# Kernel optimization log

Measured on AMD Instinct MI355X. Metric: run time of the kernel, lower is better.

Reference implementation:

```python
import jax, jax.numpy as jnp
import numpy as np

D_IN, H, V = 512, 1024, 32000
S, B, T = 64, 128, 48
MARGIN = 0.1


def setup_inputs() -> dict:
    key = jax.random.key(0)
    ks = jax.random.split(key, 16)
    sc = 0.05
    f = lambda k, shp: jax.random.normal(k, shp, jnp.float32) * sc
    emb_W = f(ks[0], (V, D_IN)).at[0].set(0.0)  # padding_idx=0 row is zero
    return dict(
        ctx=jax.random.normal(ks[1], (S, B, H), jnp.float32),
        ctx_mask=jnp.ones((S, B), jnp.float32),
        y=jax.random.randint(ks[2], (T, B), 0, V),
        emb_W=emb_W,
        W_init=f(ks[3], (H, H)), b_init=jnp.zeros((H,), jnp.float32),
        W_ih0=f(ks[4], (3 * H, D_IN)), W_hh0=f(ks[5], (3 * H, H)),
        b_ih0=jnp.zeros((3 * H,), jnp.float32), b_hh0=jnp.zeros((3 * H,), jnp.float32),
        W_c2c=f(ks[6], (H, H)), W_h2c=f(ks[7], (H, H)), v_att=f(ks[8], (H,)),
        W_ih1=f(ks[9], (3 * H, H)), W_hh1=f(ks[10], (3 * H, H)),
        b_ih1=jnp.zeros((3 * H,), jnp.float32), b_hh1=jnp.zeros((3 * H,), jnp.float32),
        W_h2o=f(ks[11], (D_IN, H)), b_h2o=jnp.zeros((D_IN,), jnp.float32),
        W_out=f(ks[12], (V, D_IN)),
    )


def _gru(x, h, Wih, Whh, bih, bhh):
    # torch.nn.GRUCell math
    gi = x @ Wih.T + bih
    gh = h @ Whh.T + bhh
    ir, iz, inn = jnp.split(gi, 3, axis=-1)
    hr, hz, hn = jnp.split(gh, 3, axis=-1)
    r = jax.nn.sigmoid(ir + hr)
    z = jax.nn.sigmoid(iz + hz)
    n = jnp.tanh(inn + r * hn)
    return (1.0 - z) * n + z * h


def reference(ctx, ctx_mask, y, emb_W, W_init, b_init, W_ih0, W_hh0, b_ih0, b_hh0,
              W_c2c, W_h2c, v_att, W_ih1, W_hh1, b_ih1, b_hh1, W_h2o, b_h2o, W_out):
    # dec_init='mean_ctx': tanh(FF(masked mean over source))
    mean_ctx = ctx.sum(0) / ctx_mask.sum(0)[:, None]            # (B,H)
    h = jnp.tanh(mean_ctx @ W_init.T + b_init)                  # h0 (B,H)

    ctx_p = jnp.einsum('sbc,dc->sbd', ctx, W_c2c)               # ctx2ctx, hoisted out of loop
    neg = jnp.where(ctx_mask > 0, 0.0, -1e9)                    # (S,B) additive mask
    W_out_n = W_out / jnp.linalg.norm(W_out, axis=-1, keepdims=True)

    emb_in = emb_W[y[:-1]]                                      # (T-1,B,D_IN)
    targets = y[1:]                                             # (T-1,B)

    def step(h, inp):
        e, tgt = inp
        h1 = _gru(e, h, W_ih0, W_hh0, b_ih0, b_hh0)             # dec0
        # MLP attention: v^T tanh(ctx2ctx(ctx) + hid2ctx(h1))
        scores = jnp.tanh(ctx_p + (h1 @ W_h2c.T)[None]) @ v_att + neg   # (S,B)
        alpha = jax.nn.softmax(scores, axis=0)
        z_t = jnp.einsum('sb,sbc->bc', alpha, ctx)              # context (B,H)
        h2 = _gru(z_t, h1, W_ih1, W_hh1, b_ih1, b_hh1)          # dec1
        logit = jnp.tanh(h2 @ W_h2o.T + b_h2o)                  # hid2out
        logit = logit / jnp.linalg.norm(logit, axis=-1, keepdims=True)
        log_p = logit @ W_out_n.T                               # (B,V) cosine sims
        # max-margin loss, contrastive_type='max', ignore pad (tgt==0)
        s_true = jnp.take_along_axis(log_p, tgt[:, None], axis=1)
        viol = jnp.maximum(MARGIN - s_true + log_p, 0.0)
        viol = viol * (1.0 - jax.nn.one_hot(tgt, V, dtype=log_p.dtype))
        l = jnp.sum(jnp.where(tgt != 0, viol.max(-1), 0.0))
        return h2, l

    _, losses = jax.lax.scan(step, h, (emb_in, targets))
    return losses.sum()
```

## Files before the change

### kernel.cpp

```cpp
#include <hip/hip_runtime.h>
#include <math.h>

#define H    1024
#define H3   3072
#define DIN  512
#define VSZ  32000
#define SS   64
#define BB   128
#define TP   47
#define NROWS (TP*BB)
#define VCHUNKS 250
#define FMARGIN 0.1f
#define NBLK 256
#define HS   65536
#define PS(i) ((i) + ((i) >> 4))

typedef unsigned short u16;
typedef unsigned int u32;
typedef unsigned long long u64;
typedef __bf16 bf16_t;
typedef bf16_t bf16x8 __attribute__((ext_vector_type(8)));
typedef float f32x4 __attribute__((ext_vector_type(4)));
typedef u16 u16x4 __attribute__((ext_vector_type(4)));
typedef u16 u16x8 __attribute__((ext_vector_type(8)));

#define MFMA __builtin_amdgcn_mfma_f32_16x16x32_bf16

__device__ inline u16 f2bf(float f){
    unsigned b = __float_as_uint(f);
    return (u16)((b + 0x7FFFu + ((b >> 16) & 1u)) >> 16);
}
__device__ inline float bf2f(u16 u){ return __uint_as_float(((unsigned)u) << 16); }
__device__ inline float sigm(float x){ return 1.f/(1.f + expf(-x)); }

__device__ inline void stoval(float* p, float v){ *p = v; }
__device__ inline void stoval(u16* p, float v){ *p = f2bf(v); }

__device__ inline void cstore(u32* p, u32 v){ __hip_atomic_store(p, v, __ATOMIC_RELAXED, __HIP_MEMORY_SCOPE_AGENT); }
__device__ inline void cstore64(u64* p, u64 v){ __hip_atomic_store(p, v, __ATOMIC_RELAXED, __HIP_MEMORY_SCOPE_AGENT); }
__device__ inline float cloadf(const float* p){ return __hip_atomic_load(p, __ATOMIC_RELAXED, __HIP_MEMORY_SCOPE_AGENT); }

__device__ inline void gbar(u32* bar, u32* mygen, int tid, int bid){
    __syncthreads();
    if (tid == 0){
        u32 tgt = ++(*mygen);
        __builtin_amdgcn_s_waitcnt(0);
        u32* cnt = bar + 64 + (bid >> 3)*32;
        u32 old = __hip_atomic_fetch_add(cnt, 1u, __ATOMIC_RELAXED, __HIP_MEMORY_SCOPE_AGENT);
        if (old == 7u){
            __hip_atomic_store(cnt, 0u, __ATOMIC_RELAXED, __HIP_MEMORY_SCOPE_AGENT);
            u32 old2 = __hip_atomic_fetch_add(&bar[1], 1u, __ATOMIC_RELEASE, __HIP_MEMORY_SCOPE_AGENT);
            if (old2 == 31u){
                __hip_atomic_store(&bar[1], 0u, __ATOMIC_RELAXED, __HIP_MEMORY_SCOPE_AGENT);
                __hip_atomic_store(&bar[0], tgt, __ATOMIC_RELEASE, __HIP_MEMORY_SCOPE_AGENT);
            }
        }
        while (__hip_atomic_load(&bar[0], __ATOMIC_RELAXED, __HIP_MEMORY_SCOPE_AGENT) < tgt)
            __builtin_amdgcn_s_sleep(1);
    }
    __syncthreads();
    asm volatile("" ::: "memory");
}


__global__ __launch_bounds__(128) void k_mask_sum(const float* __restrict__ mask, float* __restrict__ msum){
    int b = threadIdx.x;
    if (b < BB){ float s = 0.f; for (int i = 0; i < SS; i++) s += mask[i*BB + b]; msum[b] = s; }
}

__global__ __launch_bounds__(256) void k_mean_ctx(const float* __restrict__ ctx, const float* __restrict__ msum,
                                                  float* __restrict__ mean){
    int idx = blockIdx.x*256 + threadIdx.x;
    if (idx < BB*H){
        float s = 0.f;
        for (int i = 0; i < SS; i++) s += ctx[(size_t)i*BB*H + idx];
        mean[idx] = s / msum[idx / H];
    }
}

__global__ __launch_bounds__(256) void k_f32bf(const float* __restrict__ in, u16* __restrict__ out, int n4){
    int i = blockIdx.x*256 + threadIdx.x;
    if (i >= n4) return;
    float4 v = ((const float4*)in)[i];
    u16x4 o = { f2bf(v.x), f2bf(v.y), f2bf(v.z), f2bf(v.w) };
    ((u16x4*)out)[i] = o;
}

__global__ __launch_bounds__(256) void k_pack_h0(const float* __restrict__ h0, u32* __restrict__ hsHI,
                                                 u32* __restrict__ hsLO){
    int i = blockIdx.x*256 + threadIdx.x;
    float v0 = h0[i*2], v1 = h0[i*2 + 1];
    u16 a = f2bf(v0), b = f2bf(v1);
    hsHI[i] = (u32)a | ((u32)b << 16);
    hsLO[i] = (u32)f2bf(v0 - bf2f(a)) | ((u32)f2bf(v1 - bf2f(b)) << 16);
}

__global__ __launch_bounds__(256) void k_f2bf_frag(const float* __restrict__ in, u16* __restrict__ out,
                                                   int RK8, int K8){
    int t = blockIdx.x*256 + threadIdx.x;
    if (t >= RK8) return;
    int r = t / K8, k8 = t - r*K8;
    const float* p = in + (size_t)r*K8*8 + k8*8;
    float4 a = *(const float4*)p;
    float4 b = *(const float4*)(p + 4);
    size_t dst = ((size_t)(r >> 4)*(K8 >> 2) + (k8 >> 2))*512 + (size_t)((r & 15) + (k8 & 3)*16)*8;
    u16x8 o;
    o[0]=f2bf(a.x); o[1]=f2bf(a.y); o[2]=f2bf(a.z); o[3]=f2bf(a.w);
    o[4]=f2bf(b.x); o[5]=f2bf(b.y); o[6]=f2bf(b.z); o[7]=f2bf(b.w);
    *(u16x8*)(out + dst) = o;
}

__global__ __launch_bounds__(256) void k_rownorm_frag(const float* __restrict__ in, u16* __restrict__ out,
                                                      int nrows){
    int w = threadIdx.x >> 6, lane = threadIdx.x & 63;
    int row = blockIdx.x*4 + w;
    if (row >= nrows) return;
    const float* r = in + (size_t)row*512 + lane*8;
    float4 a = *(const float4*)r;
    float4 b = *(const float4*)(r + 4);
    float s = a.x*a.x + a.y*a.y + a.z*a.z + a.w*a.w
            + b.x*b.x + b.y*b.y + b.z*b.z + b.w*b.w;
    #pragma unroll
    for (int off = 32; off; off >>= 1) s += __shfl_xor(s, off);
    float inv = rsqrtf(s);
    size_t dst = ((size_t)(row >> 4)*16 + (lane >> 2))*512 + (size_t)((row & 15) + (lane & 3)*16)*8;
    u16x8 o;
    o[0]=f2bf(a.x*inv); o[1]=f2bf(a.y*inv); o[2]=f2bf(a.z*inv); o[3]=f2bf(a.w*inv);
    o[4]=f2bf(b.x*inv); o[5]=f2bf(b.y*inv); o[6]=f2bf(b.z*inv); o[7]=f2bf(b.w*inv);
    *(u16x8*)(out + dst) = o;
}

__global__ __launch_bounds__(256) void k_emb_frag(const float* __restrict__ emb, const int* __restrict__ y,
                                                  u16* __restrict__ out){
    int w = threadIdx.x >> 6, lane = threadIdx.x & 63;
    int row = blockIdx.x*4 + w;
    int src = y[row];
    const float* r = emb + (size_t)src*512 + lane*8;
    float4 a = *(const float4*)r;
    float4 b = *(const float4*)(r + 4);
    size_t dst = ((size_t)(row >> 4)*16 + (lane >> 2))*512 + (size_t)((row & 15) + (lane & 3)*16)*8;
    u16x8 o;
    o[0]=f2bf(a.x); o[1]=f2bf(a.y); o[2]=f2bf(a.z); o[3]=f2bf(a.w);
    o[4]=f2bf(b.x); o[5]=f2bf(b.y); o[6]=f2bf(b.z); o[7]=f2bf(b.w);
    *(u16x8*)(out + dst) = o;
}

template<int ACT>
__global__ __launch_bounds__(256) void k_gemm_nt(const float* __restrict__ A, const float* __restrict__ W,
                                                 const float* __restrict__ bias, float* __restrict__ C,
                                                 int M, int N, int K){
    __shared__ float As[16][68];
    __shared__ float Ws[16][68];
    int tid = threadIdx.x;
    int bm = blockIdx.y*64, bn = blockIdx.x*64;
    int lr = tid >> 2;
    int lk = (tid & 3) * 4;
    int tr = (tid >> 4) * 4;
    int tc = (tid & 15) * 4;
    float acc[4][4] = {};
    const float* Abase = A + (size_t)(bm + lr)*K;
    const float* Wbase = W + (size_t)(bn + lr)*K;
    for (int k0 = 0; k0 < K; k0 += 16){
        float4 av = *(const float4*)(Abase + k0 + lk);
        float4 wv = *(const float4*)(Wbase + k0 + lk);
        __syncthreads();
        As[lk+0][lr]=av.x; As[lk+1][lr]=av.y; As[lk+2][lr]=av.z; As[lk+3][lr]=av.w;
        Ws[lk+0][lr]=wv.x; Ws[lk+1][lr]=wv.y; Ws[lk+2][lr]=wv.z; Ws[lk+3][lr]=wv.w;
        __syncthreads();
        #pragma unroll
        for (int kk = 0; kk < 16; kk++){
            float4 a = *(const float4*)&As[kk][tr];
            float4 w = *(const float4*)&Ws[kk][tc];
            acc[0][0] += a.x*w.x; acc[0][1] += a.x*w.y; acc[0][2] += a.x*w.z; acc[0][3] += a.x*w.w;
            acc[1][0] += a.y*w.x; acc[1][1] += a.y*w.y; acc[1][2] += a.y*w.z; acc[1][3] += a.y*w.w;
            acc[2][0] += a.z*w.x; acc[2][1] += a.z*w.y; acc[2][2] += a.z*w.z; acc[2][3] += a.z*w.w;
            acc[3][0] += a.w*w.x; acc[3][1] += a.w*w.y; acc[3][2] += a.w*w.z; acc[3][3] += a.w*w.w;
        }
    }
    #pragma unroll
    for (int i = 0; i < 4; i++){
        #pragma unroll
        for (int j = 0; j < 4; j++){
            float v = acc[i][j];
            if (bias) v += bias[bn + tc + j];
            if (ACT == 1) v = tanhf(v);
            C[(size_t)(bm + tr + i)*N + bn + tc + j] = v;
        }
    }
}

template<int AFRAG, int ACT, typename OutT>
__global__ __launch_bounds__(256) void k_gemmf(const u16* __restrict__ A, const u16* __restrict__ B,
                                               const float* __restrict__ bias, OutT* __restrict__ C,
                                               int M, int N, int K){
    int tid = threadIdx.x, lane = tid & 63, w = tid >> 6;
    int wm = w >> 1, wn = w & 1;
    int row0 = blockIdx.y*128 + wm*64, col0 = blockIdx.x*128 + wn*64;
    int r16 = lane & 15, kg8 = (lane >> 4)*8, rg = (lane >> 4)*4;
    int K32 = K >> 5;
    f32x4 acc[4][4] = {};
    for (int k0 = 0; k0 < K32; k0++){
        bf16x8 af[4], bfv[4];
        #pragma unroll
        for (int i = 0; i < 4; i++){
            if (AFRAG) af[i] = *(const bf16x8*)(A + (((size_t)((row0 >> 4) + i)*K32 + k0) << 9) + lane*8);
            else       af[i] = *(const bf16x8*)(A + (size_t)(row0 + i*16 + r16)*K + k0*32 + kg8);
        }
        #pragma unroll
        for (int j = 0; j < 4; j++)
            bfv[j] = *(const bf16x8*)(B + (((size_t)((col0 >> 4) + j)*K32 + k0) << 9) + lane*8);
        #pragma unroll
        for (int i = 0; i < 4; i++)
            #pragma unroll
            for (int j = 0; j < 4; j++)
                acc[i][j] = MFMA(af[i], bfv[j], acc[i][j], 0, 0, 0);
    }
    #pragma unroll
    for (int i = 0; i < 4; i++){
        #pragma unroll
        for (int j = 0; j < 4; j++){
            #pragma unroll
            for (int r = 0; r < 4; r++){
                int row = row0 + i*16 + rg + r;
                int col = col0 + j*16 + r16;
                float v = acc[i][j][r];
                if (bias) v += bias[col];
                if (ACT) v = tanhf(v);
                stoval(C + (size_t)row*N + col, v);
            }
        }
    }
}

struct RH {
    const u16 *gi0, *Whh0, *Wh2c, *Wih1, *Whh1, *ctxp;
    const float *bhh0, *bih1, *bhh1, *vatt, *mask, *ctxf;
    u32 *hsHI, *hsLO, *h1HI, *h1LO, *ztHI, *ztLO;
    float *prF;
    float *ghF;
    u16 *h2all;
    u32 *bar;
};

__global__ __launch_bounds__(512) void k_recur7(RH a){
    __shared__ u16 wlds[49152];
    __shared__ float ps[1088];
    __shared__ float vattL[1088];
    __shared__ float sal[SS];
    __shared__ float zred[4][512];
    const int tid = threadIdx.x, lane = tid & 63, wv = tid >> 6;
    const int bid = blockIdx.x;
    const int r16 = lane & 15, rg = (lane >> 4)*4, kq4 = (lane >> 4)*4;
    const int ab = (bid & 7)*16 + ((bid >> 3) >> 1);
    const int ahalf = (bid >> 3) & 1;
    u32 mygen = 0;

    {
        auto cp32k = [&](const u16* gsrc, int tile, int base){
            const u32* s = (const u32*)(gsrc + (size_t)tile*16384);
            u32* d = (u32*)(wlds + base);
            #pragma unroll
            for (int i = 0; i < 16; i++) d[tid + i*512] = s[tid + i*512];
        };
        if (bid < 64){
            cp32k(a.Whh0, bid, 0); cp32k(a.Whh0, 64+bid, 16384); cp32k(a.Whh0, 128+bid, 32768);
        } else if (bid < 128){
            int jt = bid - 64;
            cp32k(a.Wih1, jt, 0); cp32k(a.Wih1, 64+jt, 16384); cp32k(a.Wih1, 128+jt, 32768);
        } else if (bid < 192){
            int wt = bid - 128;
            cp32k(a.Whh1, 3*wt, 0); cp32k(a.Whh1, 3*wt+1, 16384); cp32k(a.Whh1, 3*wt+2, 32768);
        } else {
            cp32k(a.Wh2c, bid-192, 0);
        }
        for (int i = tid; i < H; i += 512) vattL[PS(i)] = a.vatt[i];
    }
    __syncthreads();

    auto pf_ctxp = [&](){
        u32 acc = 0;
        #pragma unroll
        for (int i = 0; i < 4; i++){
            int line = tid + i*512;
            int s = line >> 5, l = line & 31;
            acc += *((const u32*)(a.ctxp + ((size_t)(s*BB + ab))*H) + l*16);
        }
        asm volatile("" :: "v"(acc));
    };

    for (int t = 0; t < TP; t++){
        float* prT = a.prF + (size_t)t*BB*H;

        if (bid < 64){
            const u32* AbH = a.hsHI + (size_t)t*HS + (size_t)(wv*16 + r16)*512 + kq4;
            const u32* AbL = a.hsLO + (size_t)t*HS + (size_t)(wv*16 + r16)*512 + kq4;
            f32x4 ac0 = {}, ac1 = {}, ac2 = {};
            for (int k0 = 0; k0 < 32; k0++){
                bf16x8 ah = *(const bf16x8*)(AbH + k0*16);
                bf16x8 al = *(const bf16x8*)(AbL + k0*16);
                bf16x8 b0 = *(const bf16x8*)(wlds + (k0*64 + lane)*8);
                bf16x8 b1 = *(const bf16x8*)(wlds + 16384 + (k0*64 + lane)*8);
                bf16x8 b2 = *(const bf16x8*)(wlds + 32768 + (k0*64 + lane)*8);
                ac0 = MFMA(ah, b0, ac0, 0, 0, 0); ac0 = MFMA(al, b0, ac0, 0, 0, 0);
                ac1 = MFMA(ah, b1, ac1, 0, 0, 0); ac1 = MFMA(al, b1, ac1, 0, 0, 0);
                ac2 = MFMA(ah, b2, ac2, 0, 0, 0); ac2 = MFMA(al, b2, ac2, 0, 0, 0);
            }
            const u16* gi = a.gi0 + (size_t)t*BB*H3;
            const u32* hsH = a.hsHI + (size_t)t*HS;
            const u32* hsL = a.hsLO + (size_t)t*HS;
            int sh = (r16 & 1)*16;
            #pragma unroll
            for (int r = 0; r < 4; r++){
                int b = wv*16 + rg + r, j = bid*16 + r16;
                float gr = bf2f(gi[(size_t)b*H3 + j]);
                float gz = bf2f(gi[(size_t)b*H3 + H + j]);
                float gn = bf2f(gi[(size_t)b*H3 + 2*H + j]);
                float hr = ac0[r] + a.bhh0[j];
                float hz = ac1[r] + a.bhh0[H + j];
                float hn = ac2[r] + a.bhh0[2*H + j];
                u32 uh = hsH[(size_t)b*512 + (j >> 1)];
                u32 ul = hsL[(size_t)b*512 + (j >> 1)];
                float hp = bf2f((u16)(uh >> sh)) + bf2f((u16)(ul >> sh));
                float rr = sigm(gr + hr), zz = sigm(gz + hz);
                float nn = tanhf(gn + rr*hn);
                float hv = (1.f - zz)*nn + zz*hp;
                u16 hib = f2bf(hv);
                u16 lob = f2bf(hv - bf2f(hib));
                u32 hip = (u32)__shfl_xor((int)(u32)hib, 1);
                u32 lop = (u32)__shfl_xor((int)(u32)lob, 1);
                if (!(r16 & 1)){
                    cstore(a.h1HI + (size_t)t*HS + (size_t)b*512 + (j >> 1), (u32)hib | (hip << 16));
                    cstore(a.h1LO + (size_t)t*HS + (size_t)b*512 + (j >> 1), (u32)lob | (lop << 16));
                }
            }
        } else {
            pf_ctxp();
        }
        gbar(a.bar, &mygen, tid, bid);

        if (bid >= 128){
            const u32* AbH = a.h1HI + (size_t)t*HS + (size_t)(wv*16 + r16)*512 + kq4;
            const u32* AbL = a.h1LO + (size_t)t*HS + (size_t)(wv*16 + r16)*512 + kq4;
            if (bid < 192){
                int wt = bid - 128;
                f32x4 ac0 = {}, ac1 = {}, ac2 = {};
                for (int k0 = 0; k0 < 32; k0++){
                    bf16x8 ah = *(const bf16x8*)(AbH + k0*16);
                    bf16x8 al = *(const bf16x8*)(AbL + k0*16);
                    bf16x8 b0 = *(const bf16x8*)(wlds + (k0*64 + lane)*8);
                    bf16x8 b1 = *(const bf16x8*)(wlds + 16384 + (k0*64 + lane)*8);
                    bf16x8 b2 = *(const bf16x8*)(wlds + 32768 + (k0*64 + lane)*8);
                    ac0 = MFMA(ah, b0, ac0, 0, 0, 0); ac0 = MFMA(al, b0, ac0, 0, 0, 0);
                    ac1 = MFMA(ah, b1, ac1, 0, 0, 0); ac1 = MFMA(al, b1, ac1, 0, 0, 0);
                    ac2 = MFMA(ah, b2, ac2, 0, 0, 0); ac2 = MFMA(al, b2, ac2, 0, 0, 0);
                }
                #pragma unroll
                for (int r = 0; r < 4; r++){
                    int b = wv*16 + rg + r;
                    int c0 = wt*48 + r16;
                    float p0 = __shfl_xor(ac0[r], 1);
                    float p1 = __shfl_xor(ac1[r], 1);
                    float p2 = __shfl_xor(ac2[r], 1);
                    if (!(r16 & 1)){
                        cstore64((u64*)(a.ghF + (size_t)b*H3 + c0),
                                 (u64)__float_as_uint(ac0[r]) | ((u64)__float_as_uint(p0) << 32));
                        cstore64((u64*)(a.ghF + (size_t)b*H3 + c0 + 16),
                                 (u64)__float_as_uint(ac1[r]) | ((u64)__float_as_uint(p1) << 32));
                        cstore64((u64*)(a.ghF + (size_t)b*H3 + c0 + 32),
                                 (u64)__float_as_uint(ac2[r]) | ((u64)__float_as_uint(p2) << 32));
                    }
                }
            } else {
                f32x4 ac = {};
                for (int k0 = 0; k0 < 32; k0++){
                    bf16x8 ah = *(const bf16x8*)(AbH + k0*16);
                    bf16x8 al = *(const bf16x8*)(AbL + k0*16);
                    bf16x8 bv = *(const bf16x8*)(wlds + (k0*64 + lane)*8);
                    ac = MFMA(ah, bv, ac, 0, 0, 0); ac = MFMA(al, bv, ac, 0, 0, 0);
                }
                #pragma unroll
                for (int r = 0; r < 4; r++){
                    int b = wv*16 + rg + r;
                    int c0 = (bid - 192)*16 + r16;
                    float p0 = __shfl_xor(ac[r], 1);
                    if (!(r16 & 1))
                        cstore64((u64*)(prT + (size_t)b*H + c0),
                                 (u64)__float_as_uint(ac[r]) | ((u64)__float_as_uint(p0) << 32));
                }
            }
        } else if (bid < 64){
            pf_ctxp();
        }
        gbar(a.bar, &mygen, tid, bid);

        {
            int b = ab;
            for (int i = tid; i < H; i += 512) ps[PS(i)] = prT[(size_t)b*H + i];
            __syncthreads();
            #pragma unroll
            for (int q = 0; q < 8; q += 2){
                int s0 = wv*8 + q, s1 = s0 + 1;
                const u16* cpA = a.ctxp + ((size_t)(s0*BB + b))*H + lane*16;
                const u16* cpB = a.ctxp + ((size_t)(s1*BB + b))*H + lane*16;
                u16x8 a0 = *(const u16x8*)cpA;
                u16x8 a1 = *(const u16x8*)(cpA + 8);
                u16x8 b0 = *(const u16x8*)cpB;
                u16x8 b1 = *(const u16x8*)(cpB + 8);
                const float* pp = ps + lane*17;
                const float* vv = vattL + lane*17;
                float accA = 0.f, accB = 0.f;
                #pragma unroll
                for (int e = 0; e < 8; e++){
                    accA += tanhf(bf2f(a0[e]) + pp[e]) * vv[e];
                    accB += tanhf(bf2f(b0[e]) + pp[e]) * vv[e];
                }
                #pragma unroll
                for (int e = 0; e < 8; e++){
                    accA += tanhf(bf2f(a1[e]) + pp[8 + e]) * vv[8 + e];
                    accB += tanhf(bf2f(b1[e]) + pp[8 + e]) * vv[8 + e];
                }
                #pragma unroll
                for (int off = 32; off; off >>= 1){
                    accA += __shfl_xor(accA, off);
                    accB += __shfl_xor(accB, off);
                }
                if (lane == 0){
                    sal[s0] = accA + ((a.mask[s0*BB + b] > 0.f) ? 0.f : -1e9f);
                    sal[s1] = accB + ((a.mask[s1*BB + b] > 0.f) ? 0.f : -1e9f);
                }
            }
            __syncthreads();
            if (tid < 64){
                float v = sal[tid];
                float m = v;
                #pragma unroll
                for (int off = 32; off; off >>= 1) m = fmaxf(m, __shfl_xor(m, off));
                float e = expf(v - m);
                float su = e;
                #pragma unroll
                for (int off = 32; off; off >>= 1) su += __shfl_xor(su, off);
                sal[tid] = e / su;
            }
            __syncthreads();
            int cq = (tid & 127)*4, sg = tid >> 7;
            float4 z = {0.f, 0.f, 0.f, 0.f};
            #pragma unroll
            for (int so = 0; so < 16; so += 4){
                float4 c0 = *(const float4*)(a.ctxf + ((size_t)((sg + (so+0)*4)*BB + b))*H + ahalf*512 + cq);
                float4 c1 = *(const float4*)(a.ctxf + ((size_t)((sg + (so+1)*4)*BB + b))*H + ahalf*512 + cq);
                float4 c2 = *(const float4*)(a.ctxf + ((size_t)((sg + (so+2)*4)*BB + b))*H + ahalf*512 + cq);
                float4 c3 = *(const float4*)(a.ctxf + ((size_t)((sg + (so+3)*4)*BB + b))*H + ahalf*512 + cq);
                float l0 = sal[sg + (so+0)*4], l1 = sal[sg + (so+1)*4];
                float l2 = sal[sg + (so+2)*4], l3 = sal[sg + (so+3)*4];
                z.x += l0*c0.x + l1*c1.x + l2*c2.x + l3*c3.x;
                z.y += l0*c0.y + l1*c1.y + l2*c2.y + l3*c3.y;
                z.z += l0*c0.z + l1*c1.z + l2*c2.z + l3*c3.z;
                z.w += l0*c0.w + l1*c1.w + l2*c2.w + l3*c3.w;
            }
            *(float4*)&zred[sg][cq] = z;
            __syncthreads();
            if (tid < 256){
                int c2 = tid*2;
                float a0 = zred[0][c2]   + zred[1][c2]   + zred[2][c2]   + zred[3][c2];
                float a1 = zred[0][c2+1] + zred[1][c2+1] + zred[2][c2+1] + zred[3][c2+1];
                int j0 = ahalf*512 + c2;
                u16 z0 = f2bf(a0), z1 = f2bf(a1);
                cstore(a.ztHI + (size_t)t*HS + (size_t)b*512 + (j0 >> 1), (u32)z0 | ((u32)z1 << 16));
                cstore(a.ztLO + (size_t)t*HS + (size_t)b*512 + (j0 >> 1),
                       (u32)f2bf(a0 - bf2f(z0)) | ((u32)f2bf(a1 - bf2f(z1)) << 16));
            }
            __syncthreads();
        }
        gbar(a.bar, &mygen, tid, bid);

        if (bid >= 64 && bid < 128){
            int jt = bid - 64;
            const u32* AbH = a.ztHI + (size_t)t*HS + (size_t)(wv*16 + r16)*512 + kq4;
            const u32* AbL = a.ztLO + (size_t)t*HS + (size_t)(wv*16 + r16)*512 + kq4;
            f32x4 ac0 = {}, ac1 = {}, ac2 = {};
            for (int k0 = 0; k0 < 32; k0++){
                bf16x8 ah = *(const bf16x8*)(AbH + k0*16);
                bf16x8 al = *(const bf16x8*)(AbL + k0*16);
                bf16x8 b0 = *(const bf16x8*)(wlds + (k0*64 + lane)*8);
                bf16x8 b1 = *(const bf16x8*)(wlds + 16384 + (k0*64 + lane)*8);
                bf16x8 b2 = *(const bf16x8*)(wlds + 32768 + (k0*64 + lane)*8);
                ac0 = MFMA(ah, b0, ac0, 0, 0, 0); ac0 = MFMA(al, b0, ac0, 0, 0, 0);
                ac1 = MFMA(ah, b1, ac1, 0, 0, 0); ac1 = MFMA(al, b1, ac1, 0, 0, 0);
                ac2 = MFMA(ah, b2, ac2, 0, 0, 0); ac2 = MFMA(al, b2, ac2, 0, 0, 0);
            }
            const u32* h1H = a.h1HI + (size_t)t*HS;
            const u32* h1L = a.h1LO + (size_t)t*HS;
            int sh = (r16 & 1)*16;
            #pragma unroll
            for (int r = 0; r < 4; r++){
                int b = wv*16 + rg + r, j = jt*16 + r16;
                float gr = ac0[r] + a.bih1[j];
                float gz = ac1[r] + a.bih1[H + j];
                float gn = ac2[r] + a.bih1[2*H + j];
                float hr = cloadf(a.ghF + (size_t)b*H3 + j)       + a.bhh1[j];
                float hz = cloadf(a.ghF + (size_t)b*H3 + H + j)   + a.bhh1[H + j];
                float hn = cloadf(a.ghF + (size_t)b*H3 + 2*H + j) + a.bhh1[2*H + j];
                u32 uh = h1H[(size_t)b*512 + (j >> 1)];
                u32 ul = h1L[(size_t)b*512 + (j >> 1)];
                float h1v = bf2f((u16)(uh >> sh)) + bf2f((u16)(ul >> sh));
                float rr = sigm(gr + hr), zz = sigm(gz + hz);
                float nn = tanhf(gn + rr*hn);
                float hv = (1.f - zz)*nn + zz*h1v;
                a.h2all[((size_t)t*BB + b)*H + j] = f2bf(hv);
                u16 hib = f2bf(hv);
                u16 lob = f2bf(hv - bf2f(hib));
                u32 hip = (u32)__shfl_xor((int)(u32)hib, 1);
                u32 lop = (u32)__shfl_xor((int)(u32)lob, 1);
                if (!(r16 & 1)){
                    cstore(a.hsHI + (size_t)(t+1)*HS + (size_t)b*512 + (j >> 1), (u32)hib | (hip << 16));
                    cstore(a.hsLO + (size_t)(t+1)*HS + (size_t)b*512 + (j >> 1), (u32)lob | (lop << 16));
                }
            }
        }
        gbar(a.bar, &mygen, tid, bid);
    }
}

__global__ __launch_bounds__(256) void k_final(const u16* __restrict__ logitf, const u16* __restrict__ Wf,
                                               const int* __restrict__ y, float* __restrict__ pmax,
                                               float* __restrict__ strue){
    __shared__ float red[128][2];
    int tid = threadIdx.x, w = tid >> 6, lane = tid & 63;
    int wm = w >> 1, wn = w & 1;
    int row0 = blockIdx.x*128 + wm*64;
    int col0 = blockIdx.y*128 + wn*64;
    int r16 = lane & 15, rg = (lane >> 4)*4;
    f32x4 acc[4][4] = {};
    for (int k0 = 0; k0 < 16; k0++){
        bf16x8 af[4], bfv[4];
        #pragma unroll
        for (int i = 0; i < 4; i++)
            af[i] = *(const bf16x8*)(logitf + (((size_t)((row0 >> 4) + i)*16 + k0) << 9) + lane*8);
        #pragma unroll
        for (int j = 0; j < 4; j++)
            bfv[j] = *(const bf16x8*)(Wf + (((size_t)((col0 >> 4) + j)*16 + k0) << 9) + lane*8);
        #pragma unroll
        for (int i = 0; i < 4; i++)
            #pragma unroll
            for (int j = 0; j < 4; j++)
                acc[i][j] = MFMA(af[i], bfv[j], acc[i][j], 0, 0, 0);
    }
    #pragma unroll
    for (int i = 0; i < 4; i++){
        #pragma unroll
        for (int r = 0; r < 4; r++){
            int row = row0 + i*16 + rg + r;
            int tgt = y[row + BB];
            float m = -1e30f;
            #pragma unroll
            for (int j = 0; j < 4; j++){
                float v = acc[i][j][r];
                int col = col0 + j*16 + r16;
                if (col == tgt){ strue[row] = v; v = -1e30f; }
                m = fmaxf(m, v);
            }
            m = fmaxf(m, __shfl_xor(m, 1));
            m = fmaxf(m, __shfl_xor(m, 2));
            m = fmaxf(m, __shfl_xor(m, 4));
            m = fmaxf(m, __shfl_xor(m, 8));
            if (r16 == 0) red[wm*64 + i*16 + rg + r][wn] = m;
        }
    }
    __syncthreads();
    if (tid < 128){
        float m = fmaxf(red[tid][0], red[tid][1]);
        pmax[(size_t)(blockIdx.x*128 + tid)*VCHUNKS + blockIdx.y] = m;
    }
}

__global__ __launch_bounds__(256) void k_loss(const float* __restrict__ pmax, const float* __restrict__ strue,
                                              const int* __restrict__ y, float* __restrict__ out){
    int R = blockIdx.x*256 + threadIdx.x;
    int lane = threadIdx.x & 63, wave = threadIdx.x >> 6;
    float l = 0.f;
    if (R < NROWS){
        int tgt = y[R + BB];
        if (tgt != 0){
            const float* pm = pmax + (size_t)R*VCHUNKS;
            float m = -1e30f;
            for (int i = 0; i < VCHUNKS; i++) m = fmaxf(m, pm[i]);
            l = fmaxf(FMARGIN - strue[R] + m, 0.f);
        }
    }
    #pragma unroll
    for (int off = 32; off; off >>= 1) l += __shfl_down(l, off);
    __shared__ float wsum[4];
    if (lane == 0) wsum[wave] = l;
    __syncthreads();
    if (threadIdx.x == 0) atomicAdd(out, wsum[0] + wsum[1] + wsum[2] + wsum[3]);
}

extern "C" void kernel_launch(void* const* d_in, const int* in_sizes, int n_in,
                              void* d_out, int out_size, void* d_ws, size_t ws_size,
                              hipStream_t stream){
    const float* ctx    = (const float*)d_in[0];
    const float* mask   = (const float*)d_in[1];
    const int*   y      = (const int*)d_in[2];
    const float* emb_W  = (const float*)d_in[3];
    const float* W_init = (const float*)d_in[4];
    const float* b_init = (const float*)d_in[5];
    const float* W_ih0  = (const float*)d_in[6];
    const float* W_hh0  = (const float*)d_in[7];
    const float* b_ih0  = (const float*)d_in[8];
    const float* b_hh0  = (const float*)d_in[9];
    const float* W_c2c  = (const float*)d_in[10];
    const float* W_h2c  = (const float*)d_in[11];
    const float* v_att  = (const float*)d_in[12];
    const float* W_ih1  = (const float*)d_in[13];
    const float* W_hh1  = (const float*)d_in[14];
    const float* b_ih1  = (const float*)d_in[15];
    const float* b_hh1  = (const float*)d_in[16];
    const float* W_h2o  = (const float*)d_in[17];
    const float* b_h2o  = (const float*)d_in[18];
    const float* W_out  = (const float*)d_in[19];
    float* out = (float*)d_out;

    char* wsb = (char*)d_ws;
    size_t off = 0;
    auto alloc = [&](size_t bytes)->void*{
        void* p = (void*)(wsb + off);
        off = (off + bytes + 255) & ~(size_t)255;
        return p;
    };
    u16* Wih0f = (u16*)alloc((size_t)H3*DIN*2);
    u16* Whh0f = (u16*)alloc((size_t)H3*H*2);
    u16* Wih1f = (u16*)alloc((size_t)H3*H*2);
    u16* Whh1f = (u16*)alloc((size_t)H3*H*2);
    u16* Wh2cf = (u16*)alloc((size_t)H*H*2);
    u16* Wc2cf = (u16*)alloc((size_t)H*H*2);
    u16* Wh2of = (u16*)alloc((size_t)DIN*H*2);
    u16* Woutf = (u16*)alloc((size_t)VSZ*DIN*2);
    u16* ctxb  = (u16*)alloc((size_t)SS*BB*H*2);
    u16* ctxpb = (u16*)alloc((size_t)SS*BB*H*2);
    u16* embf  = (u16*)alloc((size_t)NROWS*DIN*2);
    u16* gi0b  = (u16*)alloc((size_t)NROWS*H3*2);
    u16* h2allb= (u16*)alloc((size_t)NROWS*H*2);
    u32* hsHI  = (u32*)alloc((size_t)(TP+1)*HS*4);
    u32* hsLO  = (u32*)alloc((size_t)(TP+1)*HS*4);
    u32* h1HI  = (u32*)alloc((size_t)TP*HS*4);
    u32* h1LO  = (u32*)alloc((size_t)TP*HS*4);
    u32* ztHI  = (u32*)alloc((size_t)TP*HS*4);
    u32* ztLO  = (u32*)alloc((size_t)TP*HS*4);
    float* ghF = (float*)alloc((size_t)BB*H3*4);
    u32* bar   = (u32*)alloc(8192);
    float* strue  = (float*)alloc(NROWS*4);
    float* msum   = (float*)alloc(BB*4);
    float* meanc  = (float*)alloc((size_t)BB*H*4);
    float* h0f    = (float*)alloc((size_t)BB*H*4);

    float* prF = (float*)Woutf;

    float* logitf  = (float*)gi0b;
    u16*   logitfr = (u16*)(gi0b + (size_t)NROWS*DIN*2);
    float* pmax    = (float*)(gi0b + (size_t)NROWS*DIN*2 + (size_t)NROWS*DIN);

    hipMemsetAsync(d_out, 0, sizeof(float), stream);
    hipMemsetAsync(bar, 0, 8192, stream);

    hipLaunchKernelGGL(k_mask_sum, dim3(1), dim3(128), 0, stream, mask, msum);
    hipLaunchKernelGGL(k_mean_ctx, dim3(BB*H/256), dim3(256), 0, stream, ctx, msum, meanc);
    hipLaunchKernelGGL((k_gemm_nt<1>), dim3(H/64, BB/64), dim3(256), 0, stream,
                       meanc, W_init, b_init, h0f, BB, H, H);
    hipLaunchKernelGGL(k_pack_h0, dim3(HS/256), dim3(256), 0, stream, h0f, hsHI, hsLO);

    hipLaunchKernelGGL(k_f2bf_frag, dim3(H3*DIN/8/256), dim3(256), 0, stream, W_ih0, Wih0f, H3*DIN/8, DIN/8);
    hipLaunchKernelGGL(k_f2bf_frag, dim3(H3*H/8/256), dim3(256), 0, stream, W_hh0, Whh0f, H3*H/8, H/8);
    hipLaunchKernelGGL(k_f2bf_frag, dim3(H3*H/8/256), dim3(256), 0, stream, W_ih1, Wih1f, H3*H/8, H/8);
    hipLaunchKernelGGL(k_f2bf_frag, dim3(H3*H/8/256), dim3(256), 0, stream, W_hh1, Whh1f, H3*H/8, H/8);
    hipLaunchKernelGGL(k_f2bf_frag, dim3(H*H/8/256), dim3(256), 0, stream, W_h2c, Wh2cf, H*H/8, H/8);
    hipLaunchKernelGGL(k_f2bf_frag, dim3(H*H/8/256), dim3(256), 0, stream, W_c2c, Wc2cf, H*H/8, H/8);
    hipLaunchKernelGGL(k_f2bf_frag, dim3(DIN*H/8/256), dim3(256), 0, stream, W_h2o, Wh2of, DIN*H/8, H/8);
    hipLaunchKernelGGL(k_f32bf, dim3(SS*BB*H/4/256), dim3(256), 0, stream, ctx, ctxb, SS*BB*H/4);
    hipLaunchKernelGGL(k_emb_frag, dim3(NROWS/4), dim3(256), 0, stream, emb_W, y, embf);

    hipLaunchKernelGGL((k_gemmf<1,0,u16>), dim3(H3/128, NROWS/128), dim3(256), 0, stream,
                       embf, Wih0f, b_ih0, gi0b, NROWS, H3, DIN);
    hipLaunchKernelGGL((k_gemmf<0,0,u16>), dim3(H/128, SS*BB/128), dim3(256), 0, stream,
                       ctxb, Wc2cf, (const float*)nullptr, ctxpb, SS*BB, H, H);

    RH rh;
    rh.gi0 = gi0b; rh.Whh0 = Whh0f; rh.Wh2c = Wh2cf; rh.Wih1 = Wih1f; rh.Whh1 = Whh1f;
    rh.ctxp = ctxpb;
    rh.bhh0 = b_hh0; rh.bih1 = b_ih1; rh.bhh1 = b_hh1; rh.vatt = v_att; rh.mask = mask; rh.ctxf = ctx;
    rh.hsHI = hsHI; rh.hsLO = hsLO; rh.h1HI = h1HI; rh.h1LO = h1LO; rh.ztHI = ztHI; rh.ztLO = ztLO;
    rh.prF = prF; rh.ghF = ghF;
    rh.h2all = h2allb; rh.bar = bar;
    void* kp[] = { (void*)&rh };
    hipLaunchCooperativeKernel((const void*)k_recur7, dim3(NBLK), dim3(512), kp, 0, stream);

    hipLaunchKernelGGL(k_rownorm_frag, dim3(VSZ/4), dim3(256), 0, stream, W_out, Woutf, VSZ);
    hipLaunchKernelGGL((k_gemmf<0,1,float>), dim3(DIN/128, NROWS/128), dim3(256), 0, stream,
                       h2allb, Wh2of, b_h2o, logitf, NROWS, DIN, H);
    hipLaunchKernelGGL(k_rownorm_frag, dim3(NROWS/4), dim3(256), 0, stream, logitf, logitfr, NROWS);
    hipLaunchKernelGGL(k_final, dim3(NROWS/128, VSZ/128), dim3(256), 0, stream,
                       logitfr, Woutf, y, pmax, strue);
    hipLaunchKernelGGL(k_loss, dim3((NROWS + 255)/256), dim3(256), 0, stream, pmax, strue, y, out);
}
```

Measured before the change: 5.978 ms.

## Cache ctx projection slice in LDS and split attention scores across block halves

Each block now keeps its batch element's half-width slice of the projected context in LDS for 62 of 64 source positions, and holds v_att in registers. This replaces re-reading ctx_p from global memory every step and drops the prefetch-warming code. Scores are computed per half (512 columns) and written as partial sums to a global buffer, combined after an extra grid barrier per timestep. The context vector reduction is also simplified to one column per thread over all S. The cost is one more grid-wide barrier per step and more LDS use, which may lower occupancy headroom.

After: 5.126 ms. 14.2% less time.

```diff
diff --git a/kernel.cpp b/kernel.cpp
--- a/kernel.cpp
+++ b/kernel.cpp
@@ -13,7 +13,7 @@
 #define FMARGIN 0.1f
 #define NBLK 256
 #define HS   65536
-#define PS(i) ((i) + ((i) >> 4))
+#define CTXPL_S 62
 
 typedef unsigned short u16;
 typedef unsigned int u32;
@@ -37,6 +37,7 @@
 __device__ inline void stoval(u16* p, float v){ *p = f2bf(v); }
 
 __device__ inline void cstore(u32* p, u32 v){ __hip_atomic_store(p, v, __ATOMIC_RELAXED, __HIP_MEMORY_SCOPE_AGENT); }
+__device__ inline void cstoref(float* p, float v){ __hip_atomic_store(p, v, __ATOMIC_RELAXED, __HIP_MEMORY_SCOPE_AGENT); }
 __device__ inline void cstore64(u64* p, u64 v){ __hip_atomic_store(p, v, __ATOMIC_RELAXED, __HIP_MEMORY_SCOPE_AGENT); }
 __device__ inline float cloadf(const float* p){ return __hip_atomic_load(p, __ATOMIC_RELAXED, __HIP_MEMORY_SCOPE_AGENT); }
 
@@ -232,22 +233,21 @@
     }
 }
 
-struct RH {
+struct RI {
     const u16 *gi0, *Whh0, *Wh2c, *Wih1, *Whh1, *ctxp;
     const float *bhh0, *bih1, *bhh1, *vatt, *mask, *ctxf;
     u32 *hsHI, *hsLO, *h1HI, *h1LO, *ztHI, *ztLO;
     float *prF;
     float *ghF;
+    float *spar;
     u16 *h2all;
     u32 *bar;
 };
 
-__global__ __launch_bounds__(512) void k_recur7(RH a){
+__global__ __launch_bounds__(512) void k_recur8(RI a){
     __shared__ u16 wlds[49152];
-    __shared__ float ps[1088];
-    __shared__ float vattL[1088];
+    __shared__ u16 ctxpL[CTXPL_S*512];
     __shared__ float sal[SS];
-    __shared__ float zred[4][512];
     const int tid = threadIdx.x, lane = tid & 63, wv = tid >> 6;
     const int bid = blockIdx.x;
     const int r16 = lane & 15, rg = (lane >> 4)*4, kq4 = (lane >> 4)*4;
@@ -273,23 +273,23 @@
         } else {
             cp32k(a.Wh2c, bid-192, 0);
         }
-        for (int i = tid; i < H; i += 512) vattL[PS(i)] = a.vatt[i];
+        for (int i = tid; i < CTXPL_S*512/8; i += 512){
+            int s = (i*8) >> 9, h = (i*8) & 511;
+            *(u16x8*)(ctxpL + i*8) = *(const u16x8*)(a.ctxp + ((size_t)(s*BB + ab))*H + ahalf*512 + h);
+        }
+    }
+    float vv[8];
+    {
+        float4 v0 = *(const float4*)(a.vatt + ahalf*512 + lane*8);
+        float4 v1 = *(const float4*)(a.vatt + ahalf*512 + lane*8 + 4);
+        vv[0]=v0.x; vv[1]=v0.y; vv[2]=v0.z; vv[3]=v0.w;
+        vv[4]=v1.x; vv[5]=v1.y; vv[6]=v1.z; vv[7]=v1.w;
     }
     __syncthreads();
-
-    auto pf_ctxp = [&](){
-        u32 acc = 0;
-        #pragma unroll
-        for (int i = 0; i < 4; i++){
-            int line = tid + i*512;
-            int s = line >> 5, l = line & 31;
-            acc += *((const u32*)(a.ctxp + ((size_t)(s*BB + ab))*H) + l*16);
-        }
-        asm volatile("" :: "v"(acc));
-    };
 
     for (int t = 0; t < TP; t++){
         float* prT = a.prF + (size_t)t*BB*H;
+        float* spT = a.spar + (size_t)t*256*SS;
 
         if (bid < 64){
             const u32* AbH = a.hsHI + (size_t)t*HS + (size_t)(wv*16 + r16)*512 + kq4;
@@ -333,8 +333,6 @@
                     cstore(a.h1LO + (size_t)t*HS + (size_t)b*512 + (j >> 1), (u32)lob | (lop << 16));
                 }
             }
-        } else {
-            pf_ctxp();
         }
         gbar(a.bar, &mygen, tid, bid);
 
@@ -388,50 +386,37 @@
                                  (u64)__float_as_uint(ac[r]) | ((u64)__float_as_uint(p0) << 32));
                 }
             }
-        } else if (bid < 64){
-            pf_ctxp();
         }
         gbar(a.bar, &mygen, tid, bid);
 
         {
-            int b = ab;
-            for (int i = tid; i < H; i += 512) ps[PS(i)] = prT[(size_t)b*H + i];
-            __syncthreads();
-            #pragma unroll
-            for (int q = 0; q < 8; q += 2){
-                int s0 = wv*8 + q, s1 = s0 + 1;
-                const u16* cpA = a.ctxp + ((size_t)(s0*BB + b))*H + lane*16;
-                const u16* cpB = a.ctxp + ((size_t)(s1*BB + b))*H + lane*16;
-                u16x8 a0 = *(const u16x8*)cpA;
-                u16x8 a1 = *(const u16x8*)(cpA + 8);
-                u16x8 b0 = *(const u16x8*)cpB;
-                u16x8 b1 = *(const u16x8*)(cpB + 8);
-                const float* pp = ps + lane*17;
-                const float* vv = vattL + lane*17;
-                float accA = 0.f, accB = 0.f;
+            float pj[8];
+            {
+                float4 q0 = *(const float4*)(prT + (size_t)ab*H + ahalf*512 + lane*8);
+                float4 q1 = *(const float4*)(prT + (size_t)ab*H + ahalf*512 + lane*8 + 4);
+                pj[0]=q0.x; pj[1]=q0.y; pj[2]=q0.z; pj[3]=q0.w;
+                pj[4]=q1.x; pj[5]=q1.y; pj[6]=q1.z; pj[7]=q1.w;
+            }
+            #pragma unroll
+            for (int q = 0; q < 8; q++){
+                int s = wv*8 + q;
+                u16x8 cv;
+                if (s < CTXPL_S) cv = *(const u16x8*)(ctxpL + s*512 + lane*8);
+                else cv = *(const u16x8*)(a.ctxp + ((size_t)(s*BB + ab))*H + ahalf*512 + lane*8);
+                float acc = 0.f;
                 #pragma unroll
-                for (int e = 0; e < 8; e++){
-                    accA += tanhf(bf2f(a0[e]) + pp[e]) * vv[e];
-                    accB += tanhf(bf2f(b0[e]) + pp[e]) * vv[e];
-                }
+                for (int e = 0; e < 8; e++) acc += tanhf(bf2f(cv[e]) + pj[e]) * vv[e];
                 #pragma unroll
-                for (int e = 0; e < 8; e++){
-                    accA += tanhf(bf2f(a1[e]) + pp[8 + e]) * vv[8 + e];
-                    accB += tanhf(bf2f(b1[e]) + pp[8 + e]) * vv[8 + e];
-                }
-                #pragma unroll
-                for (int off = 32; off; off >>= 1){
-                    accA += __shfl_xor(accA, off);
-                    accB += __shfl_xor(accB, off);
-                }
-                if (lane == 0){
-                    sal[s0] = accA + ((a.mask[s0*BB + b] > 0.f) ? 0.f : -1e9f);
-                    sal[s1] = accB + ((a.mask[s1*BB + b] > 0.f) ? 0.f : -1e9f);
-                }
-            }
-            __syncthreads();
+                for (int off = 32; off; off >>= 1) acc += __shfl_xor(acc, off);
+                if (lane == 0) cstoref(spT + (ab*2 + ahalf)*SS + s, acc);
+            }
+        }
+        gbar(a.bar, &mygen, tid, bid);
+
+        {
             if (tid < 64){
-                float v = sal[tid];
+                float v = spT[(ab*2)*SS + tid] + spT[(ab*2 + 1)*SS + tid]
+                        + ((a.mask[tid*BB + ab] > 0.f) ? 0.f : -1e9f);
                 float m = v;
                 #pragma unroll
                 for (int off = 32; off; off >>= 1) m = fmaxf(m, __shfl_xor(m, off));
@@ -442,32 +427,19 @@
                 sal[tid] = e / su;
             }
             __syncthreads();
-            int cq = (tid & 127)*4, sg = tid >> 7;
-            float4 z = {0.f, 0.f, 0.f, 0.f};
-            #pragma unroll
-            for (int so = 0; so < 16; so += 4){
-                float4 c0 = *(const float4*)(a.ctxf + ((size_t)((sg + (so+0)*4)*BB + b))*H + ahalf*512 + cq);
-                float4 c1 = *(const float4*)(a.ctxf + ((size_t)((sg + (so+1)*4)*BB + b))*H + ahalf*512 + cq);
-                float4 c2 = *(const float4*)(a.ctxf + ((size_t)((sg + (so+2)*4)*BB + b))*H + ahalf*512 + cq);
-                float4 c3 = *(const float4*)(a.ctxf + ((size_t)((sg + (so+3)*4)*BB + b))*H + ahalf*512 + cq);
-                float l0 = sal[sg + (so+0)*4], l1 = sal[sg + (so+1)*4];
-                float l2 = sal[sg + (so+2)*4], l3 = sal[sg + (so+3)*4];
-                z.x += l0*c0.x + l1*c1.x + l2*c2.x + l3*c3.x;
-                z.y += l0*c0.y + l1*c1.y + l2*c2.y + l3*c3.y;
-                z.z += l0*c0.z + l1*c1.z + l2*c2.z + l3*c3.z;
-                z.w += l0*c0.w + l1*c1.w + l2*c2.w + l3*c3.w;
-            }
-            *(float4*)&zred[sg][cq] = z;
-            __syncthreads();
-            if (tid < 256){
-                int c2 = tid*2;
-                float a0 = zred[0][c2]   + zred[1][c2]   + zred[2][c2]   + zred[3][c2];
-                float a1 = zred[0][c2+1] + zred[1][c2+1] + zred[2][c2+1] + zred[3][c2+1];
-                int j0 = ahalf*512 + c2;
-                u16 z0 = f2bf(a0), z1 = f2bf(a1);
-                cstore(a.ztHI + (size_t)t*HS + (size_t)b*512 + (j0 >> 1), (u32)z0 | ((u32)z1 << 16));
-                cstore(a.ztLO + (size_t)t*HS + (size_t)b*512 + (j0 >> 1),
-                       (u32)f2bf(a0 - bf2f(z0)) | ((u32)f2bf(a1 - bf2f(z1)) << 16));
+            int col = tid;
+            const float* cbase = a.ctxf + (size_t)ab*H + ahalf*512 + col;
+            float z = 0.f;
+            #pragma unroll 8
+            for (int s = 0; s < SS; s++)
+                z += sal[s] * cbase[(size_t)s*BB*H];
+            float zp = __shfl_xor(z, 1);
+            if (!(tid & 1)){
+                int j0 = ahalf*512 + col;
+                u16 z0 = f2bf(z), z1 = f2bf(zp);
+                cstore(a.ztHI + (size_t)t*HS + (size_t)ab*512 + (j0 >> 1), (u32)z0 | ((u32)z1 << 16));
+                cstore(a.ztLO + (size_t)t*HS + (size_t)ab*512 + (j0 >> 1),
+                       (u32)f2bf(z - bf2f(z0)) | ((u32)f2bf(zp - bf2f(z1)) << 16));
             }
             __syncthreads();
         }
@@ -647,6 +619,7 @@
     u32* ztHI  = (u32*)alloc((size_t)TP*HS*4);
     u32* ztLO  = (u32*)alloc((size_t)TP*HS*4);
     float* ghF = (float*)alloc((size_t)BB*H3*4);
+    float* spar= (float*)alloc((size_t)TP*256*SS*4);
     u32* bar   = (u32*)alloc(8192);
     float* strue  = (float*)alloc(NROWS*4);
     float* msum   = (float*)alloc(BB*4);
@@ -683,15 +656,15 @@
     hipLaunchKernelGGL((k_gemmf<0,0,u16>), dim3(H/128, SS*BB/128), dim3(256), 0, stream,
                        ctxb, Wc2cf, (const float*)nullptr, ctxpb, SS*BB, H, H);
 
-    RH rh;
-    rh.gi0 = gi0b; rh.Whh0 = Whh0f; rh.Wh2c = Wh2cf; rh.Wih1 = Wih1f; rh.Whh1 = Whh1f;
-    rh.ctxp = ctxpb;
-    rh.bhh0 = b_hh0; rh.bih1 = b_ih1; rh.bhh1 = b_hh1; rh.vatt = v_att; rh.mask = mask; rh.ctxf = ctx;
-    rh.hsHI = hsHI; rh.hsLO = hsLO; rh.h1HI = h1HI; rh.h1LO = h1LO; rh.ztHI = ztHI; rh.ztLO = ztLO;
-    rh.prF = prF; rh.ghF = ghF;
-    rh.h2all = h2allb; rh.bar = bar;
-    void* kp[] = { (void*)&rh };
-    hipLaunchCooperativeKernel((const void*)k_recur7, dim3(NBLK), dim3(512), kp, 0, stream);
+    RI ri;
+    ri.gi0 = gi0b; ri.Whh0 = Whh0f; ri.Wh2c = Wh2cf; ri.Wih1 = Wih1f; ri.Whh1 = Whh1f;
+    ri.ctxp = ctxpb;
+    ri.bhh0 = b_hh0; ri.bih1 = b_ih1; ri.bhh1 = b_hh1; ri.vatt = v_att; ri.mask = mask; ri.ctxf = ctx;
+    ri.hsHI = hsHI; ri.hsLO = hsLO; ri.h1HI = h1HI; ri.h1LO = h1LO; ri.ztHI = ztHI; ri.ztLO = ztLO;
+    ri.prF = prF; ri.ghF = ghF; ri.spar = spar;
+    ri.h2all = h2allb; ri.bar = bar;
+    void* kp[] = { (void*)&ri };
+    hipLaunchCooperativeKernel((const void*)k_recur8, dim3(NBLK), dim3(512), kp, 0, stream);
 
     hipLaunchKernelGGL(k_rownorm_frag, dim3(VSZ/4), dim3(256), 0, stream, W_out, Woutf, VSZ);
     hipLaunchKernelGGL((k_gemmf<0,1,float>), dim3(DIN/128, NROWS/128), dim3(256), 0, stream,
```
